# Optimization experiments

Measured on AMD Instinct MI355X. Metric: run time of the kernel, lower is better.

Reference implementation:

```python
import jax, jax.numpy as jnp
import numpy as np

RF = 3          # receptive_field_size (cubic)
STRIDE = 1
TEMP = 1.0      # softmax temperature ('soft' sampling, eval mode: no Gumbel noise)
TREE_DEPTH = 4

# Truth table of all 16 binary gates: GATES[g, t] = value of gate g on input
# pattern t = 2*a + b (a = first child, b = second child), t in {0,1,2,3}.
GATES = np.array([[(g >> t) & 1 for t in range(4)] for g in range(16)],
                 dtype=np.float32)  # (16, 4)


def _lut_eval(a, b, w):
    """Differentiable 2-input LUT. a, b: (B,K,P,nodes); w: (nodes,K,16)."""
    probs = jax.nn.softmax(w / TEMP, axis=-1)          # (nodes,K,16)
    lut = probs @ jnp.asarray(GATES)                   # (nodes,K,4) relaxed truth table
    lut = jnp.moveaxis(lut, 0, 1)[:, None]             # (K,1,nodes,4) -> bcast over B,P
    l0, l1, l2, l3 = lut[..., 0], lut[..., 1], lut[..., 2], lut[..., 3]
    na, nb = 1.0 - a, 1.0 - b
    # E[lut(a,b)] under independent Bernoulli inputs
    return l0 * na * nb + l1 * na * b + l2 * a * nb + l3 * a * b


def setup_inputs() -> dict:
    key = jax.random.key(0)
    ks = jax.random.split(key, 8)
    B, C, H, W, D = 4, 3, 32, 32, 32
    K, S = 32, 16  # num_kernels, lut_rank**tree_depth leaves
    x = jax.random.uniform(ks[0], (B, C, H, W, D), dtype=jnp.float32)
    # (lut_rank=2, K, S, 4) coords (h, w, d, c); rf=3 and channels=3 so all in [0,3)
    kernel_coords = jax.random.randint(ks[1], (2, K, S, 4), 0, 3, dtype=jnp.int32)
    w0 = jax.random.normal(ks[2], (16, K, 16), dtype=jnp.float32)
    w1 = jax.random.normal(ks[3], (8, K, 16), dtype=jnp.float32)
    w2 = jax.random.normal(ks[4], (4, K, 16), dtype=jnp.float32)
    w3 = jax.random.normal(ks[5], (2, K, 16), dtype=jnp.float32)
    w4 = jax.random.normal(ks[6], (1, K, 16), dtype=jnp.float32)
    return {"x": x, "kernel_coords": kernel_coords,
            "w0": w0, "w1": w1, "w2": w2, "w3": w3, "w4": w4}


def reference(x, kernel_coords, w0, w1, w2, w3, w4):
    B, C, H, W, D = x.shape
    OH, OW, OD = (H - RF) // STRIDE + 1, (W - RF) // STRIDE + 1, (D - RF) // STRIDE + 1
    kc = kernel_coords
    # linear offset of each leaf coord inside flattened (C,H,W,D) volume
    base = ((kc[..., 3] * H + kc[..., 0]) * W + kc[..., 1]) * D + kc[..., 2]  # (2,K,S)
    oh = jnp.arange(OH) * STRIDE
    ow = jnp.arange(OW) * STRIDE
    od = jnp.arange(OD) * STRIDE
    patch = ((oh[:, None, None] * W + ow[None, :, None]) * D
             + od[None, None, :]).reshape(-1)                                  # (P,)
    lin = base[:, :, None, :] + patch[None, None, :, None]                     # (2,K,P,S)
    g = x.reshape(B, -1)[:, lin]                                               # (B,2,K,P,S)
    out = _lut_eval(g[:, 0], g[:, 1], w0)                                      # (B,K,P,S)
    for w in (w1, w2, w3, w4):  # binary tree reduction over TREE_DEPTH levels
        out = _lut_eval(out[..., 0::2], out[..., 1::2], w)
    return out.reshape(B, out.shape[1], OH, OW, OD)
```

## Files before the change

kernel.cpp:

```cpp
#include <hip/hip_runtime.h>


#define B_  4
#define C_  3
#define H_  32
#define W_  32
#define D_  32
#define K_  32
#define S_  16
#define WS  33
#define TPB 512

typedef float v8f __attribute__((ext_vector_type(8), aligned(4)));

__device__ __forceinline__ v8f lut8(v8f a, v8f b, float l0, float d1, float d2, float d3) {
    const v8f t0 = a * d2 + l0;
    const v8f t1 = a * d3 + d1;
    return b * t1 + t0;
}

__global__ __launch_bounds__(TPB, 4) void logic_conv3d(
    const float* __restrict__ x,
    const int*   __restrict__ kc,
    const float* __restrict__ w0,
    const float* __restrict__ w1,
    const float* __restrict__ w2,
    const float* __restrict__ w3,
    const float* __restrict__ w4,
    float*       __restrict__ out)
{
    __shared__ float4 s_lut[2][31];
    __shared__ __align__(16) int s_lb[2][16];
    __shared__ __align__(16) int s_gb[2][16];
    __shared__ __align__(16) float slab[18 * 32 * WS];

    const int bx  = blockIdx.x;
    const int b   = bx >> 4;
    const int k0  = (bx & 15) << 1;
    const int tid = threadIdx.x;
    const int oh0 = blockIdx.y * 4;

    if (tid < 62) {
        const int kk   = (tid >= 31) ? 1 : 0;
        const int node = tid - kk * 31;
        const int k    = k0 + kk;
        const float* wp; int ln;
        if      (node < 16) { wp = w0; ln = node;      }
        else if (node < 24) { wp = w1; ln = node - 16; }
        else if (node < 28) { wp = w2; ln = node - 24; }
        else if (node < 30) { wp = w3; ln = node - 28; }
        else                { wp = w4; ln = 0;         }
        const float* wrow = wp + (ln * K_ + k) * 16;
        float lg[16];
        float m = -1e30f;
        #pragma unroll
        for (int g = 0; g < 16; ++g) { lg[g] = wrow[g]; m = fmaxf(m, lg[g]); }
        float z = 0.f;
        #pragma unroll
        for (int g = 0; g < 16; ++g) { lg[g] = __expf(lg[g] - m); z += lg[g]; }
        const float inv = 1.0f / z;
        float l0 = 0.f, l1 = 0.f, l2 = 0.f, l3 = 0.f;
        #pragma unroll
        for (int g = 0; g < 16; ++g) {
            float p = lg[g] * inv;
            if (g & 1) l0 += p;
            if (g & 2) l1 += p;
            if (g & 4) l2 += p;
            if (g & 8) l3 += p;
        }
        s_lut[kk][node] = make_float4(l0, l1 - l0, l2 - l0, (l3 - l2) - (l1 - l0));
    } else if (tid >= 64 && tid < 128) {
        const int idx  = tid - 64;
        const int kk   = idx >> 5;
        const int tree = (idx >> 4) & 1;
        const int s    = idx & 15;
        const int k    = k0 + kk;
        const int off  = ((tree * K_ + k) * S_ + s) * 4;
        const int h = kc[off + 0], w = kc[off + 1], d = kc[off + 2], c = kc[off + 3];
        if (tree == 0)
            s_lb[kk][s] = ((c * 6 + h) * 32 + w) * WS + d;
        else
            s_gb[kk][s] = ((c * H_ + h) * W_ + w) * D_ + d;
    }

    {
        const float* xb = x + (size_t)b * (C_ * H_ * W_ * D_);
        #pragma unroll
        for (int it = 0; it < 9; ++it) {
            const int idx   = it * TPB + tid;
            const int plane = idx >> 8;
            const int f4    = idx & 255;
            const int c     = plane / 6;
            const int dh    = plane - c * 6;
            const int h     = min(oh0 + dh, H_ - 1);
            const int w     = f4 >> 3;
            const int d4    = (f4 & 7) << 2;
            const float4 val = *(const float4*)(xb + ((c * H_ + h) * W_ + w) * D_ + d4);
            *(float4*)&slab[(plane * 32 + w) * WS + d4] = val;
        }
    }
    __syncthreads();

    const int ohl = tid >> 7;
    const int r   = tid & 127;
    const int ow  = r >> 2;
    const int gq  = r & 3;
    const int od0 = (gq < 3) ? (gq << 3) : 22;
    const int oh  = oh0 + ohl;

    if (ow < 30 && oh < 30) {
        const int vo  = ohl * (32 * WS) + ow * WS + od0;
        const int gvo = ohl * (W_ * D_) + ow * D_ + od0;
        const float* xg = x + (size_t)b * (C_ * H_ * W_ * D_) + oh0 * (W_ * D_);

        #pragma unroll
        for (int kk = 0; kk < 2; ++kk) {
            int sA[16], sB[16];
            #pragma unroll
            for (int i = 0; i < 4; ++i) {
                const int4 qa = *(const int4*)&s_lb[kk][i * 4];
                sA[i * 4 + 0] = __builtin_amdgcn_readfirstlane(qa.x);
                sA[i * 4 + 1] = __builtin_amdgcn_readfirstlane(qa.y);
                sA[i * 4 + 2] = __builtin_amdgcn_readfirstlane(qa.z);
                sA[i * 4 + 3] = __builtin_amdgcn_readfirstlane(qa.w);
                const int4 qb = *(const int4*)&s_gb[kk][i * 4];
                sB[i * 4 + 0] = __builtin_amdgcn_readfirstlane(qb.x);
                sB[i * 4 + 1] = __builtin_amdgcn_readfirstlane(qb.y);
                sB[i * 4 + 2] = __builtin_amdgcn_readfirstlane(qb.z);
                sB[i * 4 + 3] = __builtin_amdgcn_readfirstlane(qb.w);
            }

            v8f v1[8];
            #pragma unroll
            for (int j = 0; j < 8; ++j) {
                const int s0 = 2 * j, s1 = 2 * j + 1;
                const v8f A0 = *(const v8f*)&slab[sA[s0] + vo];
                const v8f B0 = *(const v8f*)(xg + sB[s0] + gvo);
                const float4 L0 = s_lut[kk][s0];
                const v8f t0 = lut8(A0, B0, L0.x, L0.y, L0.z, L0.w);
                const v8f A1 = *(const v8f*)&slab[sA[s1] + vo];
                const v8f B1 = *(const v8f*)(xg + sB[s1] + gvo);
                const float4 L1 = s_lut[kk][s1];
                const v8f t1 = lut8(A1, B1, L1.x, L1.y, L1.z, L1.w);
                const float4 LN = s_lut[kk][16 + j];
                v1[j] = lut8(t0, t1, LN.x, LN.y, LN.z, LN.w);
            }

            #pragma unroll
            for (int j = 0; j < 4; ++j) {
                const float4 L = s_lut[kk][24 + j];
                v1[j] = lut8(v1[2 * j], v1[2 * j + 1], L.x, L.y, L.z, L.w);
            }
            #pragma unroll
            for (int j = 0; j < 2; ++j) {
                const float4 L = s_lut[kk][28 + j];
                v1[j] = lut8(v1[2 * j], v1[2 * j + 1], L.x, L.y, L.z, L.w);
            }
            {
                const float4 L = s_lut[kk][30];
                v1[0] = lut8(v1[0], v1[1], L.x, L.y, L.z, L.w);
            }

            const int bk = b * K_ + k0 + kk;
            float* outp = out + (size_t)bk * 27000 + oh * 900 + ow * 30 + od0;
            *(v8f*)outp = v1[0];
        }
    }
}

extern "C" void kernel_launch(void* const* d_in, const int* in_sizes, int n_in,
                              void* d_out, int out_size, void* d_ws, size_t ws_size,
                              hipStream_t stream) {
    const float* x  = (const float*)d_in[0];
    const int*   kc = (const int*)d_in[1];
    const float* w0 = (const float*)d_in[2];
    const float* w1 = (const float*)d_in[3];
    const float* w2 = (const float*)d_in[4];
    const float* w3 = (const float*)d_in[5];
    const float* w4 = (const float*)d_in[6];
    float* out = (float*)d_out;

    dim3 grid((B_ * K_) / 2, 8);
    logic_conv3d<<<grid, TPB, 0, stream>>>(x, kc, w0, w1, w2, w3, w4, out);
}
```

Measured before the change: 82.24 us.

## Halve output rows per block and vector width to raise parallelism

```diff
diff --git a/kernel.cpp b/kernel.cpp
--- a/kernel.cpp
+++ b/kernel.cpp
@@ -11,15 +11,15 @@
 #define WS  33
 #define TPB 512
 
-typedef float v8f __attribute__((ext_vector_type(8), aligned(4)));
+typedef float v4f __attribute__((ext_vector_type(4), aligned(4)));
 
-__device__ __forceinline__ v8f lut8(v8f a, v8f b, float l0, float d1, float d2, float d3) {
-    const v8f t0 = a * d2 + l0;
-    const v8f t1 = a * d3 + d1;
+__device__ __forceinline__ v4f lut4(v4f a, v4f b, float l0, float d1, float d2, float d3) {
+    const v4f t0 = a * d2 + l0;
+    const v4f t1 = a * d3 + d1;
     return b * t1 + t0;
 }
 
-__global__ __launch_bounds__(TPB, 4) void logic_conv3d(
+__global__ __launch_bounds__(TPB, 6) void logic_conv3d(
     const float* __restrict__ x,
     const int*   __restrict__ kc,
     const float* __restrict__ w0,
@@ -32,13 +32,13 @@
     __shared__ float4 s_lut[2][31];
     __shared__ __align__(16) int s_lb[2][16];
     __shared__ __align__(16) int s_gb[2][16];
-    __shared__ __align__(16) float slab[18 * 32 * WS];
+    __shared__ __align__(16) float slab[12 * 32 * WS];
 
     const int bx  = blockIdx.x;
     const int b   = bx >> 4;
     const int k0  = (bx & 15) << 1;
     const int tid = threadIdx.x;
-    const int oh0 = blockIdx.y * 4;
+    const int oh0 = blockIdx.y * 2;
 
     if (tid < 62) {
         const int kk   = (tid >= 31) ? 1 : 0;
@@ -78,7 +78,7 @@
         const int off  = ((tree * K_ + k) * S_ + s) * 4;
         const int h = kc[off + 0], w = kc[off + 1], d = kc[off + 2], c = kc[off + 3];
         if (tree == 0)
-            s_lb[kk][s] = ((c * 6 + h) * 32 + w) * WS + d;
+            s_lb[kk][s] = ((c * 4 + h) * 32 + w) * WS + d;
         else
             s_gb[kk][s] = ((c * H_ + h) * W_ + w) * D_ + d;
     }
@@ -86,13 +86,13 @@
     {
         const float* xb = x + (size_t)b * (C_ * H_ * W_ * D_);
         #pragma unroll
-        for (int it = 0; it < 9; ++it) {
+        for (int it = 0; it < 6; ++it) {
             const int idx   = it * TPB + tid;
             const int plane = idx >> 8;
             const int f4    = idx & 255;
-            const int c     = plane / 6;
-            const int dh    = plane - c * 6;
-            const int h     = min(oh0 + dh, H_ - 1);
+            const int c     = plane >> 2;
+            const int dh    = plane & 3;
+            const int h     = oh0 + dh;
             const int w     = f4 >> 3;
             const int d4    = (f4 & 7) << 2;
             const float4 val = *(const float4*)(xb + ((c * H_ + h) * W_ + w) * D_ + d4);
@@ -101,14 +101,14 @@
     }
     __syncthreads();
 
-    const int ohl = tid >> 7;
-    const int r   = tid & 127;
-    const int ow  = r >> 2;
-    const int gq  = r & 3;
-    const int od0 = (gq < 3) ? (gq << 3) : 22;
+    const int ohl = tid >> 8;
+    const int r   = tid & 255;
+    const int ow  = r >> 3;
+    const int q   = r & 7;
+    const int od0 = (q < 7) ? (q << 2) : 26;
     const int oh  = oh0 + ohl;
 
-    if (ow < 30 && oh < 30) {
+    if (ow < 30) {
         const int vo  = ohl * (32 * WS) + ow * WS + od0;
         const int gvo = ohl * (W_ * D_) + ow * D_ + od0;
         const float* xg = x + (size_t)b * (C_ * H_ * W_ * D_) + oh0 * (W_ * D_);
@@ -130,40 +130,40 @@
                 sB[i * 4 + 3] = __builtin_amdgcn_readfirstlane(qb.w);
             }
 
-            v8f v1[8];
+            v4f v1[8];
             #pragma unroll
             for (int j = 0; j < 8; ++j) {
                 const int s0 = 2 * j, s1 = 2 * j + 1;
-                const v8f A0 = *(const v8f*)&slab[sA[s0] + vo];
-                const v8f B0 = *(const v8f*)(xg + sB[s0] + gvo);
+                const v4f A0 = *(const v4f*)&slab[sA[s0] + vo];
+                const v4f B0 = *(const v4f*)(xg + sB[s0] + gvo);
                 const float4 L0 = s_lut[kk][s0];
-                const v8f t0 = lut8(A0, B0, L0.x, L0.y, L0.z, L0.w);
-                const v8f A1 = *(const v8f*)&slab[sA[s1] + vo];
-                const v8f B1 = *(const v8f*)(xg + sB[s1] + gvo);
+                const v4f t0 = lut4(A0, B0, L0.x, L0.y, L0.z, L0.w);
+                const v4f A1 = *(const v4f*)&slab[sA[s1] + vo];
+                const v4f B1 = *(const v4f*)(xg + sB[s1] + gvo);
                 const float4 L1 = s_lut[kk][s1];
-                const v8f t1 = lut8(A1, B1, L1.x, L1.y, L1.z, L1.w);
+                const v4f t1 = lut4(A1, B1, L1.x, L1.y, L1.z, L1.w);
                 const float4 LN = s_lut[kk][16 + j];
-                v1[j] = lut8(t0, t1, LN.x, LN.y, LN.z, LN.w);
+                v1[j] = lut4(t0, t1, LN.x, LN.y, LN.z, LN.w);
             }
 
             #pragma unroll
             for (int j = 0; j < 4; ++j) {
                 const float4 L = s_lut[kk][24 + j];
-                v1[j] = lut8(v1[2 * j], v1[2 * j + 1], L.x, L.y, L.z, L.w);
+                v1[j] = lut4(v1[2 * j], v1[2 * j + 1], L.x, L.y, L.z, L.w);
             }
             #pragma unroll
             for (int j = 0; j < 2; ++j) {
                 const float4 L = s_lut[kk][28 + j];
-                v1[j] = lut8(v1[2 * j], v1[2 * j + 1], L.x, L.y, L.z, L.w);
+                v1[j] = lut4(v1[2 * j], v1[2 * j + 1], L.x, L.y, L.z, L.w);
             }
             {
                 const float4 L = s_lut[kk][30];
-                v1[0] = lut8(v1[0], v1[1], L.x, L.y, L.z, L.w);
+                v1[0] = lut4(v1[0], v1[1], L.x, L.y, L.z, L.w);
             }
 
             const int bk = b * K_ + k0 + kk;
             float* outp = out + (size_t)bk * 27000 + oh * 900 + ow * 30 + od0;
-            *(v8f*)outp = v1[0];
+            *(v4f*)outp = v1[0];
         }
     }
 }
@@ -180,6 +180,6 @@
     const float* w4 = (const float*)d_in[6];
     float* out = (float*)d_out;
 
-    dim3 grid((B_ * K_) / 2, 8);
+    dim3 grid((B_ * K_) / 2, 15);
     logic_conv3d<<<grid, TPB, 0, stream>>>(x, kc, w0, w1, w2, w3, w4, out);
 }
```

Measured after the change: 82.41 us. No clear change (+0.2%).
